# Kernel tuning notes

Measured on AMD Instinct MI355X. Metric: run time of the kernel, lower is better.

## Reference

```python
import jax, jax.numpy as jnp
import numpy as np

N_NODES = 50000
N_EDGES = 800000
IN_CH = 256
OUT_CH = 64
HEADS = 4


def setup_inputs() -> dict:
    key = jax.random.key(0)
    k1, k2, k3, k4, k5 = jax.random.split(key, 5)
    x = jax.random.normal(k1, (N_NODES, IN_CH), dtype=jnp.float32)
    edge_index = jax.random.randint(k2, (2, N_EDGES), 0, N_NODES, dtype=jnp.int64)
    # xavier-ish scaled params
    weight = jax.random.normal(k3, (HEADS, IN_CH, OUT_CH), dtype=jnp.float32) * (2.0 / (IN_CH + OUT_CH)) ** 0.5
    att_src = jax.random.normal(k4, (1, HEADS, OUT_CH), dtype=jnp.float32) * 0.1
    att_dst = jax.random.normal(k5, (1, HEADS, OUT_CH), dtype=jnp.float32) * 0.1
    bias = jnp.zeros((HEADS * OUT_CH,), dtype=jnp.float32)
    return {"x": x, "edge_index": edge_index, "weight": weight,
            "att_src": att_src, "att_dst": att_dst, "bias": bias}


def reference(x, edge_index, weight, att_src, att_dst, bias):
    # GATConv forward (eval mode: dropout is identity), vectorized over heads.
    num_nodes = x.shape[0]
    row, col = edge_index[0], edge_index[1]
    # per-head projection: [N, H, C]
    x_h = jnp.einsum('nf,hfc->nhc', x, weight)
    alpha_src = jnp.sum(x_h * att_src[0], axis=-1)   # [N, H]
    alpha_dst = jnp.sum(x_h * att_dst[0], axis=-1)   # [N, H]
    alpha = alpha_src[row] + alpha_dst[col]          # [E, H]
    alpha = jax.nn.leaky_relu(alpha, negative_slope=0.2)
    # segment softmax over edges grouped by destination row (numerically stable)
    alpha_max = jax.ops.segment_max(alpha, row, num_segments=num_nodes)  # [N, H]
    alpha = jnp.exp(alpha - alpha_max[row])
    alpha_sum = jax.ops.segment_sum(alpha, row, num_segments=num_nodes)  # [N, H]
    alpha = alpha / jnp.clip(alpha_sum[row], 1e-16)
    # message passing: scatter-add alpha-weighted source features
    messages = alpha[:, :, None] * x_h[col]                              # [E, H, C]
    out = jax.ops.segment_sum(messages, row, num_segments=num_nodes)    # [N, H, C]
    out = out.reshape(num_nodes, -1) + bias                              # concat heads
    return out
```

## Files before the change

### kernel.cpp

```cpp
#include <hip/hip_runtime.h>
#include <hip/hip_fp16.h>
#include <math.h>

#define N_IN_CH 256
#define N_OUT   256
#define HEADS   4
#define OUT_CH  64
#define BM      64
#define HM      32
#define SCAN_BLOCK 1024

typedef __attribute__((ext_vector_type(8))) short bf16x8;
typedef __attribute__((ext_vector_type(4))) float f32x4;

__device__ __forceinline__ float lrelu(float a) {
  return a >= 0.f ? a : 0.2f * a;
}

__device__ __forceinline__ ushort f2bf(float f) {
  uint u = __float_as_uint(f);
  uint r = (u + 0x7FFFu + ((u >> 16) & 1u)) >> 16;
  return (ushort)r;
}

__device__ __forceinline__ ushort f2h(float f) {
  return __half_as_ushort(__float2half(f));
}
__device__ __forceinline__ float h2f(ushort u) {
  return __half2float(__ushort_as_half(u));
}

__device__ __forceinline__ int wave_scan_partials(const int* __restrict__ partials,
                                                  int nparts, int lane) {
  int pv = (lane < nparts) ? partials[lane] : 0;
  int incl = pv;
#pragma unroll
  for (int d = 1; d < 64; d <<= 1) {
    int t = __shfl_up(incl, d, 64);
    if (lane >= d) incl += t;
  }
  return incl - pv;
}

__global__ void convert_w(const float* __restrict__ w, ushort* __restrict__ bt,
                          int* __restrict__ counts, int nnodes) {
  const int idx = blockIdx.x * 256 + threadIdx.x;
  if (idx < nnodes) counts[idx] = 0;
  const int n = idx >> 8, k = idx & 255;
  const int h = n >> 6, c = n & 63;
  bt[idx] = f2bf(w[h * (N_IN_CH * OUT_CH) + k * OUT_CH + c]);
}

__global__ __launch_bounds__(256) void proj_count(
    const float* __restrict__ x, const ushort* __restrict__ bt,
    const float* __restrict__ att_src, const float* __restrict__ att_dst,
    ushort* __restrict__ xh, float* __restrict__ asrc, float* __restrict__ adst,
    int nnodes, int nblocksA,
    const int* __restrict__ row, int* __restrict__ counts,
    int* __restrict__ rank, int nedges) {
  __shared__ ushort at[HM * N_IN_CH];
  const int tid = threadIdx.x;
  const int bid = blockIdx.x;
  const int g = bid / 5;
  const bool is_proj = (bid % 5 == 0) && (g < nblocksA);

  if (!is_proj) {
    const int cb = (bid % 5 == 0) ? (4 * g)
                                  : (4 * g + (bid % 5) - 1);
    const int e = cb * 256 + tid;
    if (e < nedges) rank[e] = atomicAdd(&counts[row[e]], 1);
    return;
  }

  const int wave = tid >> 6;
  const int lane = tid & 63;
  const int lmod = lane & 15;
  const int ldiv = lane >> 4;

  float atts[4], attd[4];
#pragma unroll
  for (int nt = 0; nt < 4; ++nt) {
    const int gcol = wave * 64 + nt * 16 + lmod;
    atts[nt] = att_src[gcol];
    attd[nt] = att_dst[gcol];
  }

  for (int h0 = 0; h0 < 2; ++h0) {
    const int n0 = g * BM + h0 * HM;

    {
      const int rsub = tid >> 6;
      const int cf = (tid & 63) * 4;
      const int cb2 = cf * 2;
#pragma unroll
      for (int it = 0; it < 8; ++it) {
        const int lr = it * 4 + rsub;
        const int grow = n0 + lr;
        float4 xv = make_float4(0.f, 0.f, 0.f, 0.f);
        if (grow < nnodes) xv = *(const float4*)&x[(size_t)grow * N_IN_CH + cf];
        ushort4 b;
        b.x = f2bf(xv.x); b.y = f2bf(xv.y); b.z = f2bf(xv.z); b.w = f2bf(xv.w);
        const int cbs = cb2 ^ ((lr & 7) << 4);
        *(ushort4*)((char*)at + lr * 512 + cbs) = b;
      }
    }
    __syncthreads();

    f32x4 acc[2][4];
#pragma unroll
    for (int mt = 0; mt < 2; ++mt)
#pragma unroll
      for (int nt = 0; nt < 4; ++nt) acc[mt][nt] = (f32x4){0.f, 0.f, 0.f, 0.f};

    for (int ks = 0; ks < 8; ++ks) {
      bf16x8 a[2], b[4];
#pragma unroll
      for (int mt = 0; mt < 2; ++mt) {
        const int lr = mt * 16 + lmod;
        const int kb = ks * 64 + ldiv * 16;
        const int cbs = kb ^ ((lr & 7) << 4);
        a[mt] = *(const bf16x8*)((const char*)at + lr * 512 + cbs);
      }
#pragma unroll
      for (int nt = 0; nt < 4; ++nt) {
        const int n = wave * 64 + nt * 16 + lmod;
        b[nt] = *(const bf16x8*)&bt[(size_t)n * N_IN_CH + ks * 32 + ldiv * 8];
      }
#pragma unroll
      for (int mt = 0; mt < 2; ++mt)
#pragma unroll
        for (int nt = 0; nt < 4; ++nt)
          acc[mt][nt] = __builtin_amdgcn_mfma_f32_16x16x32_bf16(
              a[mt], b[nt], acc[mt][nt], 0, 0, 0);
    }

#pragma unroll
    for (int mt = 0; mt < 2; ++mt) {
#pragma unroll
      for (int reg = 0; reg < 4; ++reg) {
        const int grow = n0 + mt * 16 + ldiv * 4 + reg;
        const bool ok = grow < nnodes;
        float vs = 0.f, vd = 0.f;
#pragma unroll
        for (int nt = 0; nt < 4; ++nt) {
          const float v = acc[mt][nt][reg];
          if (ok) xh[(size_t)grow * N_OUT + wave * 64 + nt * 16 + lmod] = f2h(v);
          vs = fmaf(v, atts[nt], vs);
          vd = fmaf(v, attd[nt], vd);
        }
#pragma unroll
        for (int d = 1; d < 16; d <<= 1) {
          vs += __shfl_xor(vs, d, 64);
          vd += __shfl_xor(vd, d, 64);
        }
        if (lmod == 0 && ok) {
          asrc[grow * HEADS + wave] = vs;
          adst[grow * HEADS + wave] = vd;
        }
      }
    }
    __syncthreads();
  }
}

__global__ __launch_bounds__(SCAN_BLOCK) void scan1_kernel(
    const int* __restrict__ counts, int* __restrict__ offsets,
    int* __restrict__ partials, int n) {
  __shared__ int wsum[16];
  const int tid = threadIdx.x;
  const int lane = tid & 63;
  const int wid = tid >> 6;
  const int i = blockIdx.x * SCAN_BLOCK + tid;
  int v = (i < n) ? counts[i] : 0;
  int incl = v;
#pragma unroll
  for (int d = 1; d < 64; d <<= 1) {
    int t = __shfl_up(incl, d, 64);
    if (lane >= d) incl += t;
  }
  if (lane == 63) wsum[wid] = incl;
  __syncthreads();
  if (wid == 0) {
    int wv = (lane < 16) ? wsum[lane] : 0;
#pragma unroll
    for (int d = 1; d < 16; d <<= 1) {
      int t = __shfl_up(wv, d, 64);
      if (lane >= d) wv += t;
    }
    if (lane < 16) wsum[lane] = wv;
  }
  __syncthreads();
  const int wexcl = (wid == 0) ? 0 : wsum[wid - 1];
  if (i <= n) offsets[i] = wexcl + incl - v;
  if (tid == SCAN_BLOCK - 1) partials[blockIdx.x] = wsum[15];
}

__global__ void scatter_kernel(const int* __restrict__ row, const int* __restrict__ col,
                               const int* __restrict__ rank,
                               const int* __restrict__ offsets,
                               const int* __restrict__ partials, int nparts,
                               const float* __restrict__ asrc,
                               const float* __restrict__ adst,
                               uint4* __restrict__ erec, int nedges) {
  const int lane = threadIdx.x & 63;
  const int excl = wave_scan_partials(partials, nparts, lane);
  int e = blockIdx.x * blockDim.x + threadIdx.x;
  if (e < nedges) {
    const int r = row[e];
    const int c = col[e];
    const int pos = offsets[r] + __shfl(excl, r >> 10, 64) + rank[e];
    const float4 s = *(const float4*)&asrc[r * 4];
    const float4 d = *(const float4*)&adst[c * 4];
    uint4 rec;
    rec.x = (uint)c;
    rec.y = (uint)f2h(__expf(lrelu(s.x + d.x))) |
            ((uint)f2h(__expf(lrelu(s.y + d.y))) << 16);
    rec.z = (uint)f2h(__expf(lrelu(s.z + d.z))) |
            ((uint)f2h(__expf(lrelu(s.w + d.w))) << 16);
    rec.w = 0u;
    erec[pos] = rec;
  }
}

__global__ __launch_bounds__(256) void gather_kernel(
    const int* __restrict__ offsets,
    const int* __restrict__ partials, int nparts,
    const uint4* __restrict__ erec,
    const ushort* __restrict__ xh, const float* __restrict__ bias,
    float* __restrict__ out, int nnodes) {
  __shared__ float pbuf[4][64 * 4];
  const int wv = threadIdx.x >> 6;
  const int lane = threadIdx.x & 63;
  const int n = blockIdx.x * 4 + wv;
  if (n >= nnodes) return;
  const int excl = wave_scan_partials(partials, nparts, lane);
  const int off = offsets[n] + __shfl(excl, n >> 10, 64);
  const int end = offsets[n + 1] + __shfl(excl, (n + 1) >> 10, 64);
  const int deg = end - off;
  const int half = lane >> 5;
  const int ch8 = (lane & 31) * 8;
  const int hh = (lane & 31) >> 3;

  float4 s4 = make_float4(0.f, 0.f, 0.f, 0.f);
  float a0 = 0.f, a1 = 0.f, a2 = 0.f, a3 = 0.f;
  float a4 = 0.f, a5 = 0.f, a6 = 0.f, a7 = 0.f;

  for (int b = 0; b < deg; b += 64) {
    const int cnt = min(64, deg - b);
    int cl_l = 0;
    float4 p = make_float4(0.f, 0.f, 0.f, 0.f);
    if (lane < cnt) {
      const uint4 rec = erec[off + b + lane];
      cl_l = (int)rec.x;
      p.x = h2f((ushort)(rec.y & 0xFFFFu));
      p.y = h2f((ushort)(rec.y >> 16));
      p.z = h2f((ushort)(rec.z & 0xFFFFu));
      p.w = h2f((ushort)(rec.z >> 16));
      s4.x += p.x; s4.y += p.y; s4.z += p.z; s4.w += p.w;
    }
    *(float4*)&pbuf[wv][lane * 4] = p;

    for (int j = 0; j < cnt; j += 16) {
      int cq[8];
#pragma unroll
      for (int q = 0; q < 8; ++q) cq[q] = __shfl(cl_l, j + 2 * q + half, 64);
      uint4 xq[8];
#pragma unroll
      for (int q = 0; q < 8; ++q)
        xq[q] = *(const uint4*)&xh[(size_t)cq[q] * N_OUT + ch8];

      float wq[8];
#pragma unroll
      for (int q = 0; q < 8; ++q) wq[q] = pbuf[wv][(j + 2 * q + half) * 4 + hh];

#pragma unroll
      for (int q = 0; q < 8; ++q) {
        a0 = fmaf(wq[q], h2f((ushort)(xq[q].x & 0xFFFFu)), a0);
        a1 = fmaf(wq[q], h2f((ushort)(xq[q].x >> 16)), a1);
        a2 = fmaf(wq[q], h2f((ushort)(xq[q].y & 0xFFFFu)), a2);
        a3 = fmaf(wq[q], h2f((ushort)(xq[q].y >> 16)), a3);
        a4 = fmaf(wq[q], h2f((ushort)(xq[q].z & 0xFFFFu)), a4);
        a5 = fmaf(wq[q], h2f((ushort)(xq[q].z >> 16)), a5);
        a6 = fmaf(wq[q], h2f((ushort)(xq[q].w & 0xFFFFu)), a6);
        a7 = fmaf(wq[q], h2f((ushort)(xq[q].w >> 16)), a7);
      }
    }
  }

  a0 += __shfl_xor(a0, 32, 64);
  a1 += __shfl_xor(a1, 32, 64);
  a2 += __shfl_xor(a2, 32, 64);
  a3 += __shfl_xor(a3, 32, 64);
  a4 += __shfl_xor(a4, 32, 64);
  a5 += __shfl_xor(a5, 32, 64);
  a6 += __shfl_xor(a6, 32, 64);
  a7 += __shfl_xor(a7, 32, 64);

#pragma unroll
  for (int d = 1; d < 64; d <<= 1) {
    s4.x += __shfl_xor(s4.x, d, 64);
    s4.y += __shfl_xor(s4.y, d, 64);
    s4.z += __shfl_xor(s4.z, d, 64);
    s4.w += __shfl_xor(s4.w, d, 64);
  }
  const float sh = (hh == 0) ? s4.x : (hh == 1) ? s4.y : (hh == 2) ? s4.z : s4.w;
  const float invh = 1.f / fmaxf(sh, 1e-16f);

  const int wch = ch8 + half * 4;
  const float4 b4 = *(const float4*)&bias[wch];
  float4 o;
  o.x = fmaf(half ? a4 : a0, invh, b4.x);
  o.y = fmaf(half ? a5 : a1, invh, b4.y);
  o.z = fmaf(half ? a6 : a2, invh, b4.z);
  o.w = fmaf(half ? a7 : a3, invh, b4.w);
  *(float4*)&out[(size_t)n * N_OUT + wch] = o;
}

extern "C" void kernel_launch(void* const* d_in, const int* in_sizes, int n_in,
                              void* d_out, int out_size, void* d_ws, size_t ws_size,
                              hipStream_t stream) {
  const float* x        = (const float*)d_in[0];
  const int*   edge_idx = (const int*)d_in[1];
  const float* weight   = (const float*)d_in[2];
  const float* att_src  = (const float*)d_in[3];
  const float* att_dst  = (const float*)d_in[4];
  const float* bias     = (const float*)d_in[5];
  float* out = (float*)d_out;

  const int nnodes = in_sizes[0] / N_IN_CH;
  const int nedges = in_sizes[1] / 2;
  const int* row = edge_idx;
  const int* col = edge_idx + nedges;

  char* wsb = (char*)d_ws;
  size_t woff = 0;
  auto alloc = [&](size_t bytes) -> char* {
    char* p = wsb + woff;
    woff += (bytes + 255) & ~(size_t)255;
    return p;
  };
  ushort* xh    = (ushort*)alloc((size_t)nnodes * N_OUT * sizeof(ushort));
  ushort* bt    = (ushort*)alloc((size_t)N_OUT * N_IN_CH * sizeof(ushort));
  float* asrc   = (float*)alloc((size_t)nnodes * HEADS * sizeof(float));
  float* adst   = (float*)alloc((size_t)nnodes * HEADS * sizeof(float));
  int* counts   = (int*)alloc((size_t)nnodes * sizeof(int));
  int* offsets  = (int*)alloc((size_t)(nnodes + 1) * sizeof(int));
  int* partials = (int*)alloc(256 * sizeof(int));
  int* rank     = (int*)alloc((size_t)nedges * sizeof(int));
  uint4* erec   = (uint4*)alloc((size_t)nedges * sizeof(uint4));

  convert_w<<<256, 256, 0, stream>>>(weight, bt, counts, nnodes);

  const int eblocks = (nedges + 255) / 256;
  const int nblocksA = (nnodes + BM - 1) / BM;
  const int total = nblocksA + eblocks;
  proj_count<<<total, 256, 0, stream>>>(
      x, bt, att_src, att_dst, xh, asrc, adst, nnodes, nblocksA,
      row, counts, rank, nedges);

  const int nscan = (nnodes + 1 + SCAN_BLOCK - 1) / SCAN_BLOCK;
  scan1_kernel<<<nscan, SCAN_BLOCK, 0, stream>>>(counts, offsets, partials, nnodes);

  scatter_kernel<<<eblocks, 256, 0, stream>>>(row, col, rank, offsets,
                                              partials, nscan,
                                              asrc, adst, erec, nedges);

  gather_kernel<<<(nnodes + 3) / 4, 256, 0, stream>>>(offsets, partials, nscan,
                                                      erec, xh, bias, out, nnodes);
}
```

Measured before the change: 150.1 us.

## Stage projected features through LDS for coalesced stores; fold softmax sum into gather loop

```diff
diff --git a/kernel.cpp b/kernel.cpp
--- a/kernel.cpp
+++ b/kernel.cpp
@@ -143,10 +143,8 @@
         float vs = 0.f, vd = 0.f;
 #pragma unroll
         for (int nt = 0; nt < 4; ++nt) {
-          const float v = acc[mt][nt][reg];
-          if (ok) xh[(size_t)grow * N_OUT + wave * 64 + nt * 16 + lmod] = f2h(v);
-          vs = fmaf(v, atts[nt], vs);
-          vd = fmaf(v, attd[nt], vd);
+          vs = fmaf(acc[mt][nt][reg], atts[nt], vs);
+          vd = fmaf(acc[mt][nt][reg], attd[nt], vd);
         }
 #pragma unroll
         for (int d = 1; d < 16; d <<= 1) {
@@ -158,6 +156,26 @@
           adst[grow * HEADS + wave] = vd;
         }
       }
+    }
+
+    __syncthreads();
+#pragma unroll
+    for (int mt = 0; mt < 2; ++mt)
+#pragma unroll
+      for (int reg = 0; reg < 4; ++reg) {
+        const int lrow = mt * 16 + ldiv * 4 + reg;
+#pragma unroll
+        for (int nt = 0; nt < 4; ++nt)
+          at[lrow * N_OUT + wave * 64 + nt * 16 + lmod] = f2h(acc[mt][nt][reg]);
+      }
+    __syncthreads();
+#pragma unroll
+    for (int it2 = 0; it2 < 4; ++it2) {
+      const int flat = it2 * 2048 + tid * 8;
+      const int grow = n0 + (flat >> 8);
+      if (grow < nnodes)
+        *(uint4*)&xh[(size_t)grow * N_OUT + (flat & 255)] =
+            *(const uint4*)&at[flat];
     }
     __syncthreads();
   }
@@ -241,7 +259,7 @@
   const int ch8 = (lane & 31) * 8;
   const int hh = (lane & 31) >> 3;
 
-  float4 s4 = make_float4(0.f, 0.f, 0.f, 0.f);
+  float wsum = 0.f;
   float a0 = 0.f, a1 = 0.f, a2 = 0.f, a3 = 0.f;
   float a4 = 0.f, a5 = 0.f, a6 = 0.f, a7 = 0.f;
 
@@ -256,7 +274,6 @@
       p.y = h2f((ushort)(rec.y >> 16));
       p.z = h2f((ushort)(rec.z & 0xFFFFu));
       p.w = h2f((ushort)(rec.z >> 16));
-      s4.x += p.x; s4.y += p.y; s4.z += p.z; s4.w += p.w;
     }
     *(float4*)&pbuf[wv][lane * 4] = p;
 
@@ -275,6 +292,7 @@
 
 #pragma unroll
       for (int q = 0; q < 8; ++q) {
+        wsum += wq[q];
         a0 = fmaf(wq[q], h2f((ushort)(xq[q].x & 0xFFFFu)), a0);
         a1 = fmaf(wq[q], h2f((ushort)(xq[q].x >> 16)), a1);
         a2 = fmaf(wq[q], h2f((ushort)(xq[q].y & 0xFFFFu)), a2);
@@ -295,16 +313,9 @@
   a5 += __shfl_xor(a5, 32, 64);
   a6 += __shfl_xor(a6, 32, 64);
   a7 += __shfl_xor(a7, 32, 64);
-
-#pragma unroll
-  for (int d = 1; d < 64; d <<= 1) {
-    s4.x += __shfl_xor(s4.x, d, 64);
-    s4.y += __shfl_xor(s4.y, d, 64);
-    s4.z += __shfl_xor(s4.z, d, 64);
-    s4.w += __shfl_xor(s4.w, d, 64);
-  }
-  const float sh = (hh == 0) ? s4.x : (hh == 1) ? s4.y : (hh == 2) ? s4.z : s4.w;
-  const float invh = 1.f / fmaxf(sh, 1e-16f);
+  wsum += __shfl_xor(wsum, 32, 64);
+
+  const float invh = 1.f / fmaxf(wsum, 1e-16f);
 
   const int wch = ch8 + half * 4;
   const float4 b4 = *(const float4*)&bias[wch];
```

Measured after the change: 151.2 us. No clear change (+0.7%).

## Split degree-count atomics across 16 histogram slots and fold softmax sum into gather loop

Applied to the files above, without the earlier changes.

```diff
diff --git a/kernel.cpp b/kernel.cpp
--- a/kernel.cpp
+++ b/kernel.cpp
@@ -8,6 +8,7 @@
 #define OUT_CH  64
 #define BM      64
 #define HM      32
+#define NSLOT   16
 #define SCAN_BLOCK 1024
 
 typedef __attribute__((ext_vector_type(8))) short bf16x8;
@@ -42,10 +43,8 @@
   return incl - pv;
 }
 
-__global__ void convert_w(const float* __restrict__ w, ushort* __restrict__ bt,
-                          int* __restrict__ counts, int nnodes) {
+__global__ void convert_w(const float* __restrict__ w, ushort* __restrict__ bt) {
   const int idx = blockIdx.x * 256 + threadIdx.x;
-  if (idx < nnodes) counts[idx] = 0;
   const int n = idx >> 8, k = idx & 255;
   const int h = n >> 6, c = n & 63;
   bt[idx] = f2bf(w[h * (N_IN_CH * OUT_CH) + k * OUT_CH + c]);
@@ -56,7 +55,7 @@
     const float* __restrict__ att_src, const float* __restrict__ att_dst,
     ushort* __restrict__ xh, float* __restrict__ asrc, float* __restrict__ adst,
     int nnodes, int nblocksA,
-    const int* __restrict__ row, int* __restrict__ counts,
+    const int* __restrict__ row, int* __restrict__ hist,
     int* __restrict__ rank, int nedges) {
   __shared__ ushort at[HM * N_IN_CH];
   const int tid = threadIdx.x;
@@ -68,7 +67,8 @@
     const int cb = (bid % 5 == 0) ? (4 * g)
                                   : (4 * g + (bid % 5) - 1);
     const int e = cb * 256 + tid;
-    if (e < nedges) rank[e] = atomicAdd(&counts[row[e]], 1);
+    if (e < nedges)
+      rank[e] = atomicAdd(&hist[(e & (NSLOT - 1)) * nnodes + row[e]], 1);
     return;
   }
 
@@ -164,14 +164,26 @@
 }
 
 __global__ __launch_bounds__(SCAN_BLOCK) void scan1_kernel(
-    const int* __restrict__ counts, int* __restrict__ offsets,
+    int* __restrict__ hist, int* __restrict__ offsets,
     int* __restrict__ partials, int n) {
   __shared__ int wsum[16];
   const int tid = threadIdx.x;
   const int lane = tid & 63;
   const int wid = tid >> 6;
   const int i = blockIdx.x * SCAN_BLOCK + tid;
-  int v = (i < n) ? counts[i] : 0;
+
+  int v = 0;
+  if (i < n) {
+    int running = 0;
+#pragma unroll
+    for (int s = 0; s < NSLOT; ++s) {
+      const int h = hist[s * n + i];
+      hist[s * n + i] = running;
+      running += h;
+    }
+    v = running;
+  }
+
   int incl = v;
 #pragma unroll
   for (int d = 1; d < 64; d <<= 1) {
@@ -198,17 +210,19 @@
 __global__ void scatter_kernel(const int* __restrict__ row, const int* __restrict__ col,
                                const int* __restrict__ rank,
                                const int* __restrict__ offsets,
+                               const int* __restrict__ hist,
                                const int* __restrict__ partials, int nparts,
                                const float* __restrict__ asrc,
                                const float* __restrict__ adst,
-                               uint4* __restrict__ erec, int nedges) {
+                               uint4* __restrict__ erec, int nedges, int nnodes) {
   const int lane = threadIdx.x & 63;
   const int excl = wave_scan_partials(partials, nparts, lane);
   int e = blockIdx.x * blockDim.x + threadIdx.x;
   if (e < nedges) {
     const int r = row[e];
     const int c = col[e];
-    const int pos = offsets[r] + __shfl(excl, r >> 10, 64) + rank[e];
+    const int pos = offsets[r] + __shfl(excl, r >> 10, 64) +
+                    hist[(e & (NSLOT - 1)) * nnodes + r] + rank[e];
     const float4 s = *(const float4*)&asrc[r * 4];
     const float4 d = *(const float4*)&adst[c * 4];
     uint4 rec;
@@ -241,7 +255,7 @@
   const int ch8 = (lane & 31) * 8;
   const int hh = (lane & 31) >> 3;
 
-  float4 s4 = make_float4(0.f, 0.f, 0.f, 0.f);
+  float wsum = 0.f;
   float a0 = 0.f, a1 = 0.f, a2 = 0.f, a3 = 0.f;
   float a4 = 0.f, a5 = 0.f, a6 = 0.f, a7 = 0.f;
 
@@ -256,7 +270,6 @@
       p.y = h2f((ushort)(rec.y >> 16));
       p.z = h2f((ushort)(rec.z & 0xFFFFu));
       p.w = h2f((ushort)(rec.z >> 16));
-      s4.x += p.x; s4.y += p.y; s4.z += p.z; s4.w += p.w;
     }
     *(float4*)&pbuf[wv][lane * 4] = p;
 
@@ -275,6 +288,7 @@
 
 #pragma unroll
       for (int q = 0; q < 8; ++q) {
+        wsum += wq[q];
         a0 = fmaf(wq[q], h2f((ushort)(xq[q].x & 0xFFFFu)), a0);
         a1 = fmaf(wq[q], h2f((ushort)(xq[q].x >> 16)), a1);
         a2 = fmaf(wq[q], h2f((ushort)(xq[q].y & 0xFFFFu)), a2);
@@ -295,16 +309,9 @@
   a5 += __shfl_xor(a5, 32, 64);
   a6 += __shfl_xor(a6, 32, 64);
   a7 += __shfl_xor(a7, 32, 64);
-
-#pragma unroll
-  for (int d = 1; d < 64; d <<= 1) {
-    s4.x += __shfl_xor(s4.x, d, 64);
-    s4.y += __shfl_xor(s4.y, d, 64);
-    s4.z += __shfl_xor(s4.z, d, 64);
-    s4.w += __shfl_xor(s4.w, d, 64);
-  }
-  const float sh = (hh == 0) ? s4.x : (hh == 1) ? s4.y : (hh == 2) ? s4.z : s4.w;
-  const float invh = 1.f / fmaxf(sh, 1e-16f);
+  wsum += __shfl_xor(wsum, 32, 64);
+
+  const float invh = 1.f / fmaxf(wsum, 1e-16f);
 
   const int wch = ch8 + half * 4;
   const float4 b4 = *(const float4*)&bias[wch];
@@ -343,27 +350,29 @@
   ushort* bt    = (ushort*)alloc((size_t)N_OUT * N_IN_CH * sizeof(ushort));
   float* asrc   = (float*)alloc((size_t)nnodes * HEADS * sizeof(float));
   float* adst   = (float*)alloc((size_t)nnodes * HEADS * sizeof(float));
-  int* counts   = (int*)alloc((size_t)nnodes * sizeof(int));
+  int* hist     = (int*)alloc((size_t)nnodes * NSLOT * sizeof(int));
   int* offsets  = (int*)alloc((size_t)(nnodes + 1) * sizeof(int));
   int* partials = (int*)alloc(256 * sizeof(int));
   int* rank     = (int*)alloc((size_t)nedges * sizeof(int));
   uint4* erec   = (uint4*)alloc((size_t)nedges * sizeof(uint4));
 
-  convert_w<<<256, 256, 0, stream>>>(weight, bt, counts, nnodes);
+  hipMemsetAsync(hist, 0, (size_t)nnodes * NSLOT * sizeof(int), stream);
+
+  convert_w<<<256, 256, 0, stream>>>(weight, bt);
 
   const int eblocks = (nedges + 255) / 256;
   const int nblocksA = (nnodes + BM - 1) / BM;
   const int total = nblocksA + eblocks;
   proj_count<<<total, 256, 0, stream>>>(
       x, bt, att_src, att_dst, xh, asrc, adst, nnodes, nblocksA,
-      row, counts, rank, nedges);
+      row, hist, rank, nedges);
 
   const int nscan = (nnodes + 1 + SCAN_BLOCK - 1) / SCAN_BLOCK;
-  scan1_kernel<<<nscan, SCAN_BLOCK, 0, stream>>>(counts, offsets, partials, nnodes);
-
-  scatter_kernel<<<eblocks, 256, 0, stream>>>(row, col, rank, offsets,
+  scan1_kernel<<<nscan, SCAN_BLOCK, 0, stream>>>(hist, offsets, partials, nnodes);
+
+  scatter_kernel<<<eblocks, 256, 0, stream>>>(row, col, rank, offsets, hist,
                                               partials, nscan,
-                                              asrc, adst, erec, nedges);
+                                              asrc, adst, erec, nedges, nnodes);
 
   gather_kernel<<<(nnodes + 3) / 4, 256, 0, stream>>>(offsets, partials, nscan,
                                                       erec, xh, bias, out, nnodes);
```

Result: slower. 161.8 us (+7.8%).
